# Kernel tuning notes

Measured on AMD Instinct MI355X. Metric: run time of the kernel, lower is better.

Reference implementation:

```python
import jax, jax.numpy as jnp
import numpy as np

D_MODEL = 1024
NUM_HEADS = 16
D_K = D_MODEL // NUM_HEADS
NEG = -1000000000.0


def setup_inputs() -> dict:
    key = jax.random.key(0)
    ks = jax.random.split(key, 5)
    B, S = 1, 4096
    x = jax.random.normal(ks[0], (B, S, D_MODEL), dtype=jnp.float32)
    # torch nn.Linear weights are [out_features, in_features]; scale like kaiming-uniform-ish
    std = 1.0 / np.sqrt(D_MODEL)
    W_q = jax.random.normal(ks[1], (D_MODEL, D_MODEL), dtype=jnp.float32) * std
    W_k = jax.random.normal(ks[2], (D_MODEL, D_MODEL), dtype=jnp.float32) * std
    W_v = jax.random.normal(ks[3], (D_MODEL, D_MODEL), dtype=jnp.float32) * std
    W_o = jax.random.normal(ks[4], (D_MODEL, D_MODEL), dtype=jnp.float32) * std
    return {"x": x, "W_q": W_q, "W_k": W_k, "W_v": W_v, "W_o": W_o}


def reference(x, W_q, W_k, W_v, W_o):
    B, S, _ = x.shape
    scale = jnp.asarray(np.sqrt(D_K), dtype=x.dtype)
    # Linear: y = x @ W.T  (torch convention, weight [out, in])
    def proj(W):
        y = jnp.einsum('bsd,ed->bse', x, W)
        return y.reshape(B, S, NUM_HEADS, D_K).transpose(0, 2, 1, 3)  # [B,H,S,Dk]
    Q, K, V = proj(W_q), proj(W_k), proj(W_v)
    scores = jnp.einsum('bhqd,bhkd->bhqk', Q, K) / scale  # [B,H,S,S]
    causal = jnp.triu(jnp.ones((S, S), dtype=bool), k=1)  # True above diagonal
    scores = jnp.where(causal[None, None], jnp.asarray(NEG, x.dtype), scores)
    attn = jax.nn.softmax(scores, axis=-1)
    # dropout p=0.0 -> identity
    ctx = jnp.einsum('bhqk,bhkd->bhqd', attn, V)
    ctx = ctx.transpose(0, 2, 1, 3).reshape(B, S, D_MODEL)
    return jnp.einsum('bsd,ed->bse', ctx, W_o)
```

## Files before the change

kernel.cpp:

```cpp
#include <hip/hip_runtime.h>
#include <hip/hip_bf16.h>
#include <stdint.h>

#define S_LEN 4096
#define DM 1024
#define NH 16
#define DKH 64
#define LDQ (3 * DM)

typedef __attribute__((ext_vector_type(8))) __bf16 bf16x8;
typedef __attribute__((ext_vector_type(8))) short s16x8;
typedef __attribute__((ext_vector_type(4))) float f32x4;

__device__ inline unsigned short f2bf(float f) {
  unsigned int u = __builtin_bit_cast(unsigned int, f);
  u += 0x7fff + ((u >> 16) & 1);
  return (unsigned short)(u >> 16);
}
__device__ inline float bf2f(unsigned short u) {
  return __builtin_bit_cast(float, (unsigned int)u << 16);
}
__device__ inline unsigned short f2bf_hw(float f) {
  return __builtin_bit_cast(unsigned short, __float2bfloat16(f));
}

__device__ inline f32x4 mfma16(s16x8 a, s16x8 b, f32x4 c) {
  return __builtin_amdgcn_mfma_f32_16x16x32_bf16(
      __builtin_bit_cast(bf16x8, a), __builtin_bit_cast(bf16x8, b), c, 0, 0, 0);
}

__device__ inline void gld_lds16(const unsigned short* g, unsigned short* l) {
  __builtin_amdgcn_global_load_lds(
      (const __attribute__((address_space(1))) unsigned int*)g,
      (__attribute__((address_space(3))) unsigned int*)l, 16, 0, 0);
}

__global__ __launch_bounds__(256) void convert_all(
    const float* __restrict__ x, const float* __restrict__ wq,
    const float* __restrict__ wk, const float* __restrict__ wv,
    const float* __restrict__ wo, unsigned short* __restrict__ x_bf,
    unsigned short* __restrict__ wqkv, unsigned short* __restrict__ wo_bf) {
  const int XF4 = (S_LEN * DM) / 4;
  const int WF4 = (DM * DM) / 4;
  int i = blockIdx.x * blockDim.x + threadIdx.x;
  const float* src;
  unsigned short* dst;
  int off;
  if (i < XF4) { src = x; dst = x_bf; off = i; }
  else {
    int j = i - XF4;
    if (j < WF4)          { src = wq; dst = wqkv;              off = j; }
    else if (j < 2 * WF4) { src = wk; dst = wqkv + DM * DM;    off = j - WF4; }
    else if (j < 3 * WF4) { src = wv; dst = wqkv + 2 * DM * DM; off = j - 2 * WF4; }
    else                  { src = wo; dst = wo_bf;             off = j - 3 * WF4; }
  }
  float4 v = reinterpret_cast<const float4*>(src)[off];
  ushort4 o;
  o.x = f2bf(v.x); o.y = f2bf(v.y); o.z = f2bf(v.z); o.w = f2bf(v.w);
  reinterpret_cast<ushort4*>(dst)[off] = o;
}

__device__ inline void storeC(unsigned short* C, size_t i, float v) { C[i] = f2bf(v); }
__device__ inline void storeC(float* C, size_t i, float v) { C[i] = v; }

template <typename OutT>
__global__ __launch_bounds__(256) void gemm_bt(const unsigned short* __restrict__ A,
                                               const unsigned short* __restrict__ B,
                                               OutT* __restrict__ C, int M, int N, int K) {
  __shared__ __align__(16) unsigned short lds_a[128 * 64];
  __shared__ __align__(16) unsigned short lds_b[128 * 64];
  const int tid = threadIdx.x;
  const int lane = tid & 63;
  const int w = tid >> 6;
  const int wr = w >> 1, wc = w & 1;
  const int l15 = lane & 15, lhi = lane >> 4;
  const int bm0 = blockIdx.x * 128, bn0 = blockIdx.y * 128;
  const int srow = lane >> 3;
  const int scol = (lane & 7) * 8;

  f32x4 acc[4][4] = {};

  for (int k0 = 0; k0 < K; k0 += 64) {
    __syncthreads();
#pragma unroll
    for (int i = 0; i < 4; ++i) {
      const int base = i * 2048 + w * 512;
      const int row = i * 32 + w * 8 + srow;
      gld_lds16(A + (size_t)(bm0 + row) * K + k0 + scol, lds_a + base);
      gld_lds16(B + (size_t)(bn0 + row) * K + k0 + scol, lds_b + base);
    }
    __syncthreads();
#pragma unroll
    for (int kk = 0; kk < 2; ++kk) {
      s16x8 af[4], bfr[4];
#pragma unroll
      for (int mi = 0; mi < 4; ++mi)
        af[mi] = *(const s16x8*)&lds_a[(wr * 64 + mi * 16 + l15) * 64 + kk * 32 + lhi * 8];
#pragma unroll
      for (int ni = 0; ni < 4; ++ni)
        bfr[ni] = *(const s16x8*)&lds_b[(wc * 64 + ni * 16 + l15) * 64 + kk * 32 + lhi * 8];
#pragma unroll
      for (int mi = 0; mi < 4; ++mi)
#pragma unroll
        for (int ni = 0; ni < 4; ++ni)
          acc[mi][ni] = mfma16(af[mi], bfr[ni], acc[mi][ni]);
    }
  }
#pragma unroll
  for (int mi = 0; mi < 4; ++mi)
#pragma unroll
    for (int ni = 0; ni < 4; ++ni)
#pragma unroll
      for (int r = 0; r < 4; ++r) {
        int row = bm0 + wr * 64 + mi * 16 + lhi * 4 + r;
        int col = bn0 + wc * 64 + ni * 16 + l15;
        storeC(C, (size_t)row * N + col, acc[mi][ni][r]);
      }
}

__global__ __launch_bounds__(256) void transpose_v(const unsigned short* __restrict__ QKV,
                                                   unsigned short* __restrict__ vTg) {
  const int s0 = blockIdx.x * 64;
  const int h = blockIdx.y;
  __shared__ __align__(16) unsigned short t[64][72];
  const int r = threadIdx.x >> 2;
  const int c = (threadIdx.x & 3) * 16;
  const unsigned short* src = QKV + (size_t)(s0 + r) * LDQ + 2 * DM + h * DKH + c;
#pragma unroll
  for (int j = 0; j < 16; j += 4)
    *(ushort4*)&t[r][c + j] = *(const ushort4*)(src + j);
  __syncthreads();
  const int d = threadIdx.x >> 2;
  const int sc = (threadIdx.x & 3) * 16;
  unsigned short* dst = vTg + (size_t)(h * DKH + d) * S_LEN + s0 + sc;
#pragma unroll
  for (int j = 0; j < 16; j += 4) {
    ushort4 v;
    v.x = t[sc + j + 0][d]; v.y = t[sc + j + 1][d];
    v.z = t[sc + j + 2][d]; v.w = t[sc + j + 3][d];
    *(ushort4*)(dst + j) = v;
  }
}

__device__ inline void stage_kv(const unsigned short* __restrict__ Kp,
                                const unsigned short* __restrict__ vTg,
                                unsigned short* lk, unsigned short* lv,
                                int kb, int h, int tid) {
  const int w = tid >> 6, l = tid & 63;
  const int sub = l >> 3;
  const int src_col = 8 * ((l & 7) ^ sub);
#pragma unroll
  for (int i = 0; i < 2; ++i) {
    const int row = i * 32 + w * 8 + sub;
    gld_lds16(Kp + (size_t)(kb + row) * LDQ + h * DKH + src_col,
              lk + (i * 32 + w * 8) * 64);
    gld_lds16(vTg + (size_t)(h * DKH + row) * S_LEN + kb + src_col,
              lv + (i * 32 + w * 8) * 64);
  }
}

template <bool MASK>
__device__ inline void attn_tile_lds(const unsigned short* __restrict__ lk,
                                     const unsigned short* __restrict__ lv,
                                     unsigned short (*pb)[64], const s16x8 qf[2],
                                     int kb, int qrow0, int l15, int lhi,
                                     f32x4 o[4], float m_r[4], float l_r[4]) {
  const int sw = (l15 & 7) * 8;
  f32x4 sf[4];
#pragma unroll
  for (int st = 0; st < 4; ++st) {
    f32x4 acc = {};
#pragma unroll
    for (int kk = 0; kk < 2; ++kk) {
      s16x8 kf = *(const s16x8*)&lk[(st * 16 + l15) * 64 + ((kk * 32 + lhi * 8) ^ sw)];
      acc = mfma16(qf[kk], kf, acc);
    }
    sf[st] = acc;
  }
  if (MASK) {
#pragma unroll
    for (int st = 0; st < 4; ++st) {
      const int key = kb + st * 16 + l15;
#pragma unroll
      for (int r = 0; r < 4; ++r) {
        const int qrow = qrow0 + lhi * 4 + r;
        if (key > qrow) sf[st][r] = -1e30f;
      }
    }
  }
  float mt[4];
#pragma unroll
  for (int r = 0; r < 4; ++r) {
    float mx = fmaxf(fmaxf(sf[0][r], sf[1][r]), fmaxf(sf[2][r], sf[3][r]));
#pragma unroll
    for (int d = 1; d < 16; d <<= 1) mx = fmaxf(mx, __shfl_xor(mx, d));
    mt[r] = mx;
  }
  int grow = (mt[0] > m_r[0] + 8.f) | (mt[1] > m_r[1] + 8.f) |
             (mt[2] > m_r[2] + 8.f) | (mt[3] > m_r[3] + 8.f);
  const bool anyg = __any(grow);
  float alpha[4];
  if (anyg) {
#pragma unroll
    for (int r = 0; r < 4; ++r) {
      const float mn = fmaxf(m_r[r], mt[r]);
      alpha[r] = __expf(m_r[r] - mn);
      m_r[r] = mn;
    }
  }
#pragma unroll
  for (int r = 0; r < 4; ++r) {
    float rs = 0.f;
#pragma unroll
    for (int st = 0; st < 4; ++st) {
      const float p = __expf(sf[st][r] - m_r[r]);
      sf[st][r] = p;
      rs += p;
    }
#pragma unroll
    for (int d = 1; d < 16; d <<= 1) rs += __shfl_xor(rs, d);
    l_r[r] = (anyg ? l_r[r] * alpha[r] : l_r[r]) + rs;
  }
  if (anyg) {
#pragma unroll
    for (int n = 0; n < 4; ++n)
#pragma unroll
      for (int r = 0; r < 4; ++r) o[n][r] *= alpha[r];
  }
#pragma unroll
  for (int st = 0; st < 4; ++st)
#pragma unroll
    for (int r = 0; r < 4; ++r) {
      const int row = lhi * 4 + r;
      pb[row][(st * 16 + l15) ^ ((row & 7) * 8)] = f2bf_hw(sf[st][r]);
    }
#pragma unroll
  for (int kk = 0; kk < 2; ++kk) {
    s16x8 pa = *(const s16x8*)&pb[l15][(kk * 32 + lhi * 8) ^ sw];
#pragma unroll
    for (int n = 0; n < 4; ++n) {
      s16x8 vb = *(const s16x8*)&lv[(n * 16 + l15) * 64 + ((kk * 32 + lhi * 8) ^ sw)];
      o[n] = mfma16(pa, vb, o[n]);
    }
  }
}

__global__ __launch_bounds__(256, 4) void attn_split(const unsigned short* __restrict__ QKV,
                                                     const unsigned short* __restrict__ vTg,
                                                     unsigned short* __restrict__ po0,
                                                     unsigned short* __restrict__ po1,
                                                     float2* __restrict__ ml) {
  const int flat = blockIdx.x;
  const int xcd = flat & 7;
  const int t = flat >> 3;
  const int h = 2 * xcd + (t & 1);
  const int u = t >> 1;
  const int p = u & 31;
  const int b = u >> 5;
  const int tid = threadIdx.x;
  const int lane = tid & 63, w = tid >> 6;
  const int l15 = lane & 15, lhi = lane >> 4;

  __shared__ __align__(16) unsigned short lk[2][64 * 64];
  __shared__ __align__(16) unsigned short lv[2][64 * 64];
  __shared__ __align__(16) unsigned short pbuf[4][16][64];
  unsigned short (*pb)[64] = pbuf[w];

  const unsigned short* Qp = QKV;
  const unsigned short* Kp = QKV + DM;

#pragma unroll 1
  for (int mem = 0; mem < 2; ++mem) {
    const int qt  = mem ? (63 - p) : p;
    const int seg = mem ? (1 - b) : b;
    const int s0 = (qt + 2) >> 1;
    const int ks = seg ? s0 : 0;
    const int ke = seg ? (qt + 1) : s0;
    const int qrow0 = qt * 64 + w * 16;

    s16x8 qf[2];
#pragma unroll
    for (int kk = 0; kk < 2; ++kk) {
      s16x8 q = *(const s16x8*)&Qp[(size_t)(qrow0 + l15) * LDQ + h * DKH + kk * 32 + lhi * 8];
#pragma unroll
      for (int e = 0; e < 8; ++e)
        q[e] = (short)f2bf(bf2f((unsigned short)q[e]) * 0.125f);
      qf[kk] = q;
    }
    f32x4 o[4] = {};
    float m_r[4], l_r[4];
#pragma unroll
    for (int r = 0; r < 4; ++r) { m_r[r] = -1e30f; l_r[r] = 0.f; }

    __syncthreads();
    if (ks < ke) {
      stage_kv(Kp, vTg, lk[0], lv[0], ks * 64, h, tid);
      int cur = 0;
#pragma unroll 1
      for (int kbi = ks; kbi < ke; ++kbi) {
        __syncthreads();
        if (kbi + 1 < ke)
          stage_kv(Kp, vTg, lk[cur ^ 1], lv[cur ^ 1], (kbi + 1) * 64, h, tid);
        if (kbi == qt)
          attn_tile_lds<true>(lk[cur], lv[cur], pb, qf, kbi * 64, qrow0, l15, lhi, o, m_r, l_r);
        else
          attn_tile_lds<false>(lk[cur], lv[cur], pb, qf, kbi * 64, qrow0, l15, lhi, o, m_r, l_r);
        cur ^= 1;
      }
    }
    unsigned short* po = seg ? po1 : po0;
#pragma unroll
    for (int n = 0; n < 4; ++n)
#pragma unroll
      for (int r = 0; r < 4; ++r) {
        const int qrow = qrow0 + lhi * 4 + r;
        po[(size_t)qrow * DM + h * DKH + n * 16 + l15] = f2bf_hw(o[n][r]);
      }
    if (l15 == 0) {
#pragma unroll
      for (int r = 0; r < 4; ++r) {
        const int qrow = qrow0 + lhi * 4 + r;
        ml[(qrow * NH + h) * 2 + seg] = make_float2(m_r[r], l_r[r]);
      }
    }
  }
}

__global__ __launch_bounds__(256) void merge_parts(const unsigned short* __restrict__ po0,
                                                   unsigned short* __restrict__ po1_ctx,
                                                   const float2* __restrict__ ml) {
  const int i = blockIdx.x * blockDim.x + threadIdx.x;
  const int row = i >> 4, h = i & 15;
  const float2 ml0 = ml[i * 2 + 0];
  const float2 ml1 = ml[i * 2 + 1];
  const float m = fmaxf(ml0.x, ml1.x);
  const float f0 = __expf(ml0.x - m);
  const float f1 = __expf(ml1.x - m);
  const float rl = 1.f / (ml0.y * f0 + ml1.y * f1);
  const size_t base = (size_t)row * DM + h * DKH;
#pragma unroll
  for (int c = 0; c < DKH; c += 8) {
    s16x8 a = *(const s16x8*)(po0 + base + c);
    s16x8 bb = *(const s16x8*)(po1_ctx + base + c);
    s16x8 out;
#pragma unroll
    for (int j = 0; j < 8; ++j)
      out[j] = (short)f2bf_hw((bf2f((unsigned short)a[j]) * f0 +
                               bf2f((unsigned short)bb[j]) * f1) * rl);
    *(s16x8*)(po1_ctx + base + c) = out;
  }
}

extern "C" void kernel_launch(void* const* d_in, const int* in_sizes, int n_in,
                              void* d_out, int out_size, void* d_ws, size_t ws_size,
                              hipStream_t stream) {
  const float* x  = (const float*)d_in[0];
  const float* Wq = (const float*)d_in[1];
  const float* Wk = (const float*)d_in[2];
  const float* Wv = (const float*)d_in[3];
  const float* Wo = (const float*)d_in[4];
  float* out = (float*)d_out;
  char* ws = (char*)d_ws;

  unsigned short* x_bf  = (unsigned short*)(ws + 0);
  unsigned short* wqkv  = (unsigned short*)(ws + (size_t)8 * 1024 * 1024);
  unsigned short* wo_bf = (unsigned short*)(ws + (size_t)14 * 1024 * 1024);
  unsigned short* qkv   = (unsigned short*)(ws + (size_t)16 * 1024 * 1024);
  unsigned short* ctx   = (unsigned short*)(ws + (size_t)40 * 1024 * 1024);
  unsigned short* vTg   = (unsigned short*)(ws + (size_t)48 * 1024 * 1024);
  unsigned short* po0   = x_bf;
  float2*         ml    = (float2*)(ws + (size_t)8 * 1024 * 1024);

  convert_all<<<8192, 256, 0, stream>>>(x, Wq, Wk, Wv, Wo, x_bf, wqkv, wo_bf);

  dim3 g1(S_LEN / 128, (3 * DM) / 128);
  gemm_bt<unsigned short><<<g1, 256, 0, stream>>>(x_bf, wqkv, qkv, S_LEN, 3 * DM, DM);

  dim3 gt(S_LEN / 64, NH);
  transpose_v<<<gt, 256, 0, stream>>>(qkv, vTg);

  attn_split<<<1024, 256, 0, stream>>>(qkv, vTg, po0, ctx, ml);

  merge_parts<<<(S_LEN * NH) / 256, 256, 0, stream>>>(po0, ctx, ml);

  dim3 g3(S_LEN / 128, DM / 128);
  gemm_bt<float><<<g3, 256, 0, stream>>>(ctx, wo_bf, out, S_LEN, DM, DM);
}
```

Measured before the change: 294.4 us.

## Process 32 query rows per wave with transposed MFMA in attention kernel

The attention kernel drops from 4 waves of 16 query rows to 2 waves of 32 query rows each, so every K/V fragment read from LDS feeds two MFMAs. The MFMA operands are swapped to compute S^T, which makes the row max and row sum reductions need only two cross-lane shuffles and lets P and the output be written as packed 4-element vectors. The aim is to cut LDS traffic and shuffle and softmax overhead per tile. In exchange each block has half the threads, so staging does twice the loads per thread, register pressure rises, and there may be fewer waves per CU to hide latency.

```diff
diff --git a/kernel.cpp b/kernel.cpp
--- a/kernel.cpp
+++ b/kernel.cpp
@@ -49,10 +49,10 @@
   if (i < XF4) { src = x; dst = x_bf; off = i; }
   else {
     int j = i - XF4;
-    if (j < WF4)          { src = wq; dst = wqkv;              off = j; }
-    else if (j < 2 * WF4) { src = wk; dst = wqkv + DM * DM;    off = j - WF4; }
+    if (j < WF4)          { src = wq; dst = wqkv;               off = j; }
+    else if (j < 2 * WF4) { src = wk; dst = wqkv + DM * DM;     off = j - WF4; }
     else if (j < 3 * WF4) { src = wv; dst = wqkv + 2 * DM * DM; off = j - 2 * WF4; }
-    else                  { src = wo; dst = wo_bf;             off = j - 3 * WF4; }
+    else                  { src = wo; dst = wo_bf;              off = j - 3 * WF4; }
   }
   float4 v = reinterpret_cast<const float4*>(src)[off];
   ushort4 o;
@@ -150,106 +150,129 @@
   const int sub = l >> 3;
   const int src_col = 8 * ((l & 7) ^ sub);
 #pragma unroll
-  for (int i = 0; i < 2; ++i) {
-    const int row = i * 32 + w * 8 + sub;
-    gld_lds16(Kp + (size_t)(kb + row) * LDQ + h * DKH + src_col,
-              lk + (i * 32 + w * 8) * 64);
-    gld_lds16(vTg + (size_t)(h * DKH + row) * S_LEN + kb + src_col,
-              lv + (i * 32 + w * 8) * 64);
+  for (int i = 0; i < 4; ++i) {
+    const int rbase = i * 16 + w * 8;
+    const int row = rbase + sub;
+    gld_lds16(Kp + (size_t)(kb + row) * LDQ + h * DKH + src_col, lk + rbase * 64);
+    gld_lds16(vTg + (size_t)(h * DKH + row) * S_LEN + kb + src_col, lv + rbase * 64);
   }
 }
 
 template <bool MASK>
-__device__ inline void attn_tile_lds(const unsigned short* __restrict__ lk,
-                                     const unsigned short* __restrict__ lv,
-                                     unsigned short (*pb)[64], const s16x8 qf[2],
-                                     int kb, int qrow0, int l15, int lhi,
-                                     f32x4 o[4], float m_r[4], float l_r[4]) {
+__device__ inline void attn_tile2(const unsigned short* __restrict__ lk,
+                                  const unsigned short* __restrict__ lv,
+                                  unsigned short (*pb)[64], const s16x8 qf[2][2],
+                                  int kb, int qrow0, int l15, int lhi,
+                                  f32x4 o[4][2], float m_r[2], float l_r[2]) {
   const int sw = (l15 & 7) * 8;
-  f32x4 sf[4];
-#pragma unroll
-  for (int st = 0; st < 4; ++st) {
-    f32x4 acc = {};
-#pragma unroll
-    for (int kk = 0; kk < 2; ++kk) {
-      s16x8 kf = *(const s16x8*)&lk[(st * 16 + l15) * 64 + ((kk * 32 + lhi * 8) ^ sw)];
-      acc = mfma16(qf[kk], kf, acc);
-    }
-    sf[st] = acc;
-  }
+  f32x4 sf[2][4];
+#pragma unroll
+  for (int qb = 0; qb < 2; ++qb)
+#pragma unroll
+    for (int st = 0; st < 4; ++st) {
+      f32x4 acc = {};
+#pragma unroll
+      for (int kk = 0; kk < 2; ++kk) {
+        s16x8 kf = *(const s16x8*)&lk[(st * 16 + l15) * 64 + ((kk * 32 + lhi * 8) ^ sw)];
+        acc = mfma16(kf, qf[qb][kk], acc);
+      }
+      sf[qb][st] = acc;
+    }
   if (MASK) {
 #pragma unroll
+    for (int qb = 0; qb < 2; ++qb) {
+      const int qrow = qrow0 + qb * 16 + l15;
+#pragma unroll
+      for (int st = 0; st < 4; ++st)
+#pragma unroll
+        for (int r = 0; r < 4; ++r)
+          if (kb + st * 16 + lhi * 4 + r > qrow) sf[qb][st][r] = -1e30f;
+    }
+  }
+  float mt[2];
+#pragma unroll
+  for (int qb = 0; qb < 2; ++qb) {
+    float a0 = fmaxf(fmaxf(sf[qb][0][0], sf[qb][0][1]), fmaxf(sf[qb][0][2], sf[qb][0][3]));
+    float a1 = fmaxf(fmaxf(sf[qb][1][0], sf[qb][1][1]), fmaxf(sf[qb][1][2], sf[qb][1][3]));
+    float a2 = fmaxf(fmaxf(sf[qb][2][0], sf[qb][2][1]), fmaxf(sf[qb][2][2], sf[qb][2][3]));
+    float a3 = fmaxf(fmaxf(sf[qb][3][0], sf[qb][3][1]), fmaxf(sf[qb][3][2], sf[qb][3][3]));
+    float mx = fmaxf(fmaxf(a0, a1), fmaxf(a2, a3));
+    mx = fmaxf(mx, __shfl_xor(mx, 16));
+    mx = fmaxf(mx, __shfl_xor(mx, 32));
+    mt[qb] = mx;
+  }
+  const bool anyg = __any((mt[0] > m_r[0] + 8.f) | (mt[1] > m_r[1] + 8.f));
+  float alpha[2];
+  if (anyg) {
+#pragma unroll
+    for (int qb = 0; qb < 2; ++qb) {
+      const float mn = fmaxf(m_r[qb], mt[qb]);
+      alpha[qb] = __expf(m_r[qb] - mn);
+      m_r[qb] = mn;
+    }
+  }
+#pragma unroll
+  for (int qb = 0; qb < 2; ++qb) {
+    const float m = m_r[qb];
+#pragma unroll
     for (int st = 0; st < 4; ++st) {
-      const int key = kb + st * 16 + l15;
-#pragma unroll
-      for (int r = 0; r < 4; ++r) {
-        const int qrow = qrow0 + lhi * 4 + r;
-        if (key > qrow) sf[st][r] = -1e30f;
-      }
-    }
-  }
-  float mt[4];
-#pragma unroll
-  for (int r = 0; r < 4; ++r) {
-    float mx = fmaxf(fmaxf(sf[0][r], sf[1][r]), fmaxf(sf[2][r], sf[3][r]));
-#pragma unroll
-    for (int d = 1; d < 16; d <<= 1) mx = fmaxf(mx, __shfl_xor(mx, d));
-    mt[r] = mx;
-  }
-  int grow = (mt[0] > m_r[0] + 8.f) | (mt[1] > m_r[1] + 8.f) |
-             (mt[2] > m_r[2] + 8.f) | (mt[3] > m_r[3] + 8.f);
-  const bool anyg = __any(grow);
-  float alpha[4];
+      f32x4 t = sf[qb][st];
+      t[0] = __expf(t[0] - m); t[1] = __expf(t[1] - m);
+      t[2] = __expf(t[2] - m); t[3] = __expf(t[3] - m);
+      sf[qb][st] = t;
+    }
+    float s0 = (sf[qb][0][0] + sf[qb][0][1]) + (sf[qb][0][2] + sf[qb][0][3]);
+    float s1 = (sf[qb][1][0] + sf[qb][1][1]) + (sf[qb][1][2] + sf[qb][1][3]);
+    float s2 = (sf[qb][2][0] + sf[qb][2][1]) + (sf[qb][2][2] + sf[qb][2][3]);
+    float s3 = (sf[qb][3][0] + sf[qb][3][1]) + (sf[qb][3][2] + sf[qb][3][3]);
+    float rs = (s0 + s1) + (s2 + s3);
+    rs += __shfl_xor(rs, 16);
+    rs += __shfl_xor(rs, 32);
+    l_r[qb] = (anyg ? l_r[qb] * alpha[qb] : l_r[qb]) + rs;
+  }
   if (anyg) {
 #pragma unroll
-    for (int r = 0; r < 4; ++r) {
-      const float mn = fmaxf(m_r[r], mt[r]);
-      alpha[r] = __expf(m_r[r] - mn);
-      m_r[r] = mn;
-    }
-  }
-#pragma unroll
-  for (int r = 0; r < 4; ++r) {
-    float rs = 0.f;
+    for (int n = 0; n < 4; ++n)
+#pragma unroll
+      for (int qb = 0; qb < 2; ++qb) {
+        f32x4 t = o[n][qb];
+        t[0] *= alpha[qb]; t[1] *= alpha[qb]; t[2] *= alpha[qb]; t[3] *= alpha[qb];
+        o[n][qb] = t;
+      }
+  }
+#pragma unroll
+  for (int qb = 0; qb < 2; ++qb) {
+    const int row = qb * 16 + l15;
+    const int rsw = (row & 7) * 8;
 #pragma unroll
     for (int st = 0; st < 4; ++st) {
-      const float p = __expf(sf[st][r] - m_r[r]);
-      sf[st][r] = p;
-      rs += p;
-    }
-#pragma unroll
-    for (int d = 1; d < 16; d <<= 1) rs += __shfl_xor(rs, d);
-    l_r[r] = (anyg ? l_r[r] * alpha[r] : l_r[r]) + rs;
-  }
-  if (anyg) {
-#pragma unroll
-    for (int n = 0; n < 4; ++n)
-#pragma unroll
-      for (int r = 0; r < 4; ++r) o[n][r] *= alpha[r];
-  }
-#pragma unroll
-  for (int st = 0; st < 4; ++st)
-#pragma unroll
-    for (int r = 0; r < 4; ++r) {
-      const int row = lhi * 4 + r;
-      pb[row][(st * 16 + l15) ^ ((row & 7) * 8)] = f2bf_hw(sf[st][r]);
-    }
+      ushort4 pk;
+      pk.x = f2bf_hw(sf[qb][st][0]); pk.y = f2bf_hw(sf[qb][st][1]);
+      pk.z = f2bf_hw(sf[qb][st][2]); pk.w = f2bf_hw(sf[qb][st][3]);
+      *(ushort4*)&pb[row][(st * 16 + lhi * 4) ^ rsw] = pk;
+    }
+  }
 #pragma unroll
   for (int kk = 0; kk < 2; ++kk) {
-    s16x8 pa = *(const s16x8*)&pb[l15][(kk * 32 + lhi * 8) ^ sw];
+    s16x8 pa[2];
+#pragma unroll
+    for (int qb = 0; qb < 2; ++qb)
+      pa[qb] = *(const s16x8*)&pb[qb * 16 + l15][(kk * 32 + lhi * 8) ^ sw];
 #pragma unroll
     for (int n = 0; n < 4; ++n) {
       s16x8 vb = *(const s16x8*)&lv[(n * 16 + l15) * 64 + ((kk * 32 + lhi * 8) ^ sw)];
-      o[n] = mfma16(pa, vb, o[n]);
-    }
-  }
-}
-
-__global__ __launch_bounds__(256, 4) void attn_split(const unsigned short* __restrict__ QKV,
-                                                     const unsigned short* __restrict__ vTg,
-                                                     unsigned short* __restrict__ po0,
-                                                     unsigned short* __restrict__ po1,
-                                                     float2* __restrict__ ml) {
+#pragma unroll
+      for (int qb = 0; qb < 2; ++qb)
+        o[n][qb] = mfma16(vb, pa[qb], o[n][qb]);
+    }
+  }
+}
+
+__global__ __launch_bounds__(128, 2) void attn_split2(const unsigned short* __restrict__ QKV,
+                                                      const unsigned short* __restrict__ vTg,
+                                                      unsigned short* __restrict__ po0,
+                                                      unsigned short* __restrict__ po1,
+                                                      float2* __restrict__ ml) {
   const int flat = blockIdx.x;
   const int xcd = flat & 7;
   const int t = flat >> 3;
@@ -263,7 +286,7 @@
 
   __shared__ __align__(16) unsigned short lk[2][64 * 64];
   __shared__ __align__(16) unsigned short lv[2][64 * 64];
-  __shared__ __align__(16) unsigned short pbuf[4][16][64];
+  __shared__ __align__(16) unsigned short pbuf[2][32][64];
   unsigned short (*pb)[64] = pbuf[w];
 
   const unsigned short* Qp = QKV;
@@ -276,21 +299,21 @@
     const int s0 = (qt + 2) >> 1;
     const int ks = seg ? s0 : 0;
     const int ke = seg ? (qt + 1) : s0;
-    const int qrow0 = qt * 64 + w * 16;
-
-    s16x8 qf[2];
-#pragma unroll
-    for (int kk = 0; kk < 2; ++kk) {
-      s16x8 q = *(const s16x8*)&Qp[(size_t)(qrow0 + l15) * LDQ + h * DKH + kk * 32 + lhi * 8];
-#pragma unroll
-      for (int e = 0; e < 8; ++e)
-        q[e] = (short)f2bf(bf2f((unsigned short)q[e]) * 0.125f);
-      qf[kk] = q;
-    }
-    f32x4 o[4] = {};
-    float m_r[4], l_r[4];
-#pragma unroll
-    for (int r = 0; r < 4; ++r) { m_r[r] = -1e30f; l_r[r] = 0.f; }
+    const int qrow0 = qt * 64 + w * 32;
+
+    s16x8 qf[2][2];
+#pragma unroll
+    for (int qb = 0; qb < 2; ++qb)
+#pragma unroll
+      for (int kk = 0; kk < 2; ++kk) {
+        s16x8 q = *(const s16x8*)&Qp[(size_t)(qrow0 + qb * 16 + l15) * LDQ + h * DKH + kk * 32 + lhi * 8];
+#pragma unroll
+        for (int e = 0; e < 8; ++e)
+          q[e] = (short)f2bf(bf2f((unsigned short)q[e]) * 0.125f);
+        qf[qb][kk] = q;
+      }
+    f32x4 o[4][2] = {};
+    float m_r[2] = {-1e30f, -1e30f}, l_r[2] = {0.f, 0.f};
 
     __syncthreads();
     if (ks < ke) {
@@ -302,25 +325,29 @@
         if (kbi + 1 < ke)
           stage_kv(Kp, vTg, lk[cur ^ 1], lv[cur ^ 1], (kbi + 1) * 64, h, tid);
         if (kbi == qt)
-          attn_tile_lds<true>(lk[cur], lv[cur], pb, qf, kbi * 64, qrow0, l15, lhi, o, m_r, l_r);
+          attn_tile2<true>(lk[cur], lv[cur], pb, qf, kbi * 64, qrow0, l15, lhi, o, m_r, l_r);
         else
-          attn_tile_lds<false>(lk[cur], lv[cur], pb, qf, kbi * 64, qrow0, l15, lhi, o, m_r, l_r);
+          attn_tile2<false>(lk[cur], lv[cur], pb, qf, kbi * 64, qrow0, l15, lhi, o, m_r, l_r);
         cur ^= 1;
       }
     }
     unsigned short* po = seg ? po1 : po0;
 #pragma unroll
-    for (int n = 0; n < 4; ++n)
-#pragma unroll
-      for (int r = 0; r < 4; ++r) {
-        const int qrow = qrow0 + lhi * 4 + r;
-        po[(size_t)qrow * DM + h * DKH + n * 16 + l15] = f2bf_hw(o[n][r]);
-      }
-    if (l15 == 0) {
-#pragma unroll
-      for (int r = 0; r < 4; ++r) {
-        const int qrow = qrow0 + lhi * 4 + r;
-        ml[(qrow * NH + h) * 2 + seg] = make_float2(m_r[r], l_r[r]);
+    for (int qb = 0; qb < 2; ++qb) {
+      const int qrow = qrow0 + qb * 16 + l15;
+#pragma unroll
+      for (int n = 0; n < 4; ++n) {
+        ushort4 ov;
+        ov.x = f2bf_hw(o[n][qb][0]); ov.y = f2bf_hw(o[n][qb][1]);
+        ov.z = f2bf_hw(o[n][qb][2]); ov.w = f2bf_hw(o[n][qb][3]);
+        *(ushort4*)(po + (size_t)qrow * DM + h * DKH + n * 16 + lhi * 4) = ov;
+      }
+    }
+    if (lhi == 0) {
+#pragma unroll
+      for (int qb = 0; qb < 2; ++qb) {
+        const int qrow = qrow0 + qb * 16 + l15;
+        ml[(qrow * NH + h) * 2 + seg] = make_float2(m_r[qb], l_r[qb]);
       }
     }
   }
@@ -379,7 +406,7 @@
   dim3 gt(S_LEN / 64, NH);
   transpose_v<<<gt, 256, 0, stream>>>(qkv, vTg);
 
-  attn_split<<<1024, 256, 0, stream>>>(qkv, vTg, po0, ctx, ml);
+  attn_split2<<<1024, 128, 0, stream>>>(qkv, vTg, po0, ctx, ml);
 
   merge_parts<<<(S_LEN * NH) / 256, 256, 0, stream>>>(po0, ctx, ml);
 
```

After: 242.8 us. 1.21x faster.
